# Kernel tuning notes

Measured on AMD Instinct MI355X. Metric: run time of the kernel, lower is better.

Reference implementation:

```python
import jax, jax.numpy as jnp
import numpy as np

N_X, N_UNITS, N_Y, N_U = 64, 256, 32, 64
BATCH = 32768


def setup_inputs() -> dict:
    key = jax.random.key(0)
    ks = jax.random.split(key, 10)
    nz = 2 * N_X + N_UNITS
    return {
        "u": jax.random.normal(ks[0], (BATCH, N_U, 1), dtype=jnp.float32),
        "x0": jax.random.normal(ks[1], (BATCH, N_X, 1), dtype=jnp.float32),
        # learned parameters (scaled down so H stays well-conditioned and tanh unsaturated)
        "B_2": 0.1 * jax.random.normal(ks[2], (N_X, N_U), dtype=jnp.float32),
        "C_2": 0.1 * jax.random.normal(ks[3], (N_Y, N_X), dtype=jnp.float32),
        "D_12": 0.1 * jax.random.normal(ks[4], (N_UNITS, N_U), dtype=jnp.float32),
        "D_21": 0.1 * jax.random.normal(ks[5], (N_Y, N_UNITS), dtype=jnp.float32),
        "b": 0.1 * jax.random.normal(ks[6], (N_X + N_UNITS + N_Y, 1), dtype=jnp.float32),
        "X": (1.0 / np.sqrt(nz)) * jax.random.normal(ks[7], (nz, nz), dtype=jnp.float32),
        "Y1": 0.1 * jax.random.normal(ks[8], (N_X, N_X), dtype=jnp.float32),
        # fixed IQC multipliers (train_qsr=False): Q nsd, R=I so Rinv=I; S stored transposed
        "S_t": 0.1 * jax.random.normal(ks[9], (N_U, N_Y), dtype=jnp.float32),
        "Q": -jnp.eye(N_Y, dtype=jnp.float32),
        "Rinv": jnp.eye(N_U, dtype=jnp.float32),
    }


def _constrained_weights(B_2, C_2, D_12, D_21, X, S_t, Q, Rinv):
    """Port of REN.updateConstrainedWeights (train_qsr=False). Returns C_1, D_11, lam."""
    n_x, n_units = B_2.shape[0], D_12.shape[0]
    n_y = C_2.shape[0]
    nz = 2 * n_x + n_units
    C2_ = S_t @ C_2                       # [n_u, n_x]
    D21_ = S_t @ D_21 - D_12.T            # [n_u, n_units]
    H = X.T @ X + 1e-3 * jnp.eye(nz, dtype=X.dtype)
    lT1 = jnp.concatenate([C2_.T, D21_.T, B_2], axis=0)          # [nz, n_u]
    H = H + lT1 @ Rinv @ lT1.T
    lT2 = jnp.concatenate([C_2.T, D_21.T, jnp.zeros((n_x, n_y), dtype=X.dtype)], axis=0)
    H = H - lT2 @ Q @ lT2.T
    H_21 = H[n_x:n_x + n_units, :n_x]
    H_22 = H[n_x:n_x + n_units, n_x:n_x + n_units]
    C_1 = -H_21                           # [n_units, n_x]
    lam = 0.5 * jnp.diag(H_22)            # Lambda diagonal, > 0 since H is PD
    # L = tril(-(H_22 - diag(H_22))) == -strictly_lower(H_22)
    D_11 = -jnp.tril(H_22, k=-1)          # strictly lower triangular [n_units, n_units]
    return C_1, D_11, lam


def _forward(u, x0, B_2, C_2, D_12, D_21, b, X, Y1, S_t, Q, Rinv):
    n_x, n_units = B_2.shape[0], D_12.shape[0]
    C_1, D_11, lam = _constrained_weights(B_2, C_2, D_12, D_21, X, S_t, Q, Rinv)
    u2 = u[:, :, 0]                       # [B, n_u]
    x2 = x0[:, :, 0]                      # [B, n_x]
    b_w = b[n_x:n_x + n_units, 0]         # [n_units]
    b_y = b[n_x + n_units:, 0]            # [n_y]
    # precompute the non-recurrent part of the pre-activation for all units
    v = x2 @ C_1.T + u2 @ D_12.T + b_w    # [B, n_units]
    # NOTE: the source uses D_11 row (i_unit - 1), not i_unit (faithful to original code).
    # For i=0 the source uses term2 = 0; D_11 is strictly lower so the full-row dot
    # against the partially-filled w (zeros beyond index i) matches D_11[i-1, :i] @ w[:i].
    Drows = jnp.concatenate([jnp.zeros((1, n_units), dtype=D_11.dtype), D_11[:-1]], axis=0)
    batch = u2.shape[0]

    def step(w, i):
        wi = jnp.tanh((v[:, i] + w @ Drows[i]) / lam[i])   # [B]
        w = w.at[:, i].set(wi)
        return w, None

    w0 = jnp.zeros((batch, n_units), dtype=v.dtype)
    w, _ = jax.lax.scan(step, w0, jnp.arange(n_units))
    y = x2 @ C_2.T + w @ D_21.T + b_y     # [B, n_y]
    return y[:, :, None]                  # [B, n_y, 1]


def reference(u, x0, B_2, C_2, D_12, D_21, b, X, Y1, S_t, Q, Rinv):
    return _forward(u, x0, B_2, C_2, D_12, D_21, b, X, Y1, S_t, Q, Rinv)
```

## Files before the change

kernel.cpp:

```cpp
#include <hip/hip_runtime.h>
#include <hip/hip_bf16.h>

typedef __attribute__((ext_vector_type(8))) short short8;
typedef __attribute__((ext_vector_type(4))) float floatx4;
typedef __attribute__((ext_vector_type(2))) float floatx2;

#define MFMA16 __builtin_amdgcn_mfma_f32_16x16x32_bf16

__device__ inline unsigned short bf16_rn(float f) {
    return (unsigned short)((__float_as_uint(f) + 0x8000u) >> 16);
}
__device__ inline short8 pack8(const float* v) {
    union { short8 s; unsigned int u[4]; } r;
#pragma unroll
    for (int j = 0; j < 4; j++) {
        union { __hip_bfloat162 h; unsigned int u; } c;
        c.h = __float22bfloat162_rn(make_float2(v[2 * j], v[2 * j + 1]));
        r.u[j] = c.u;
    }
    return r.s;
}

__global__ __launch_bounds__(64) void ren_prep13(
    const float* __restrict__ B2, const float* __restrict__ C2,
    const float* __restrict__ D12, const float* __restrict__ D21,
    const float* __restrict__ St, const float* __restrict__ Q,
    const float* __restrict__ Rinv,
    float* __restrict__ lT1, float* __restrict__ t1,
    float* __restrict__ lT2, float* __restrict__ t2,
    unsigned short* __restrict__ Wvb, unsigned short* __restrict__ C2b,
    unsigned short* __restrict__ D21b)
{
    const int t = threadIdx.x;
    const int blk = blockIdx.x;
    if (blk >= 384) {
        const int id = (blk - 384) * 64 + t;
        if (id < 16384) {
            Wvb[(id >> 6) * 128 + 64 + (id & 63)] = bf16_rn(D12[id]);
        } else if (id < 16384 + 2048) {
            C2b[id - 16384] = bf16_rn(C2[id - 16384]);
        } else if (id < 16384 + 2048 + 8192) {
            D21b[id - 18432] = bf16_rn(D21[id - 18432]);
        }
        return;
    }

    __shared__ float stl[64 * 33];
    __shared__ float colbuf[32];
    __shared__ float s1[64];

    const int r = blk;
    const int c = t;
#pragma unroll
    for (int j = 0; j < 32; j++) {
        const int id = j * 64 + t;
        stl[(id >> 5) * 33 + (id & 31)] = St[id];
    }
    if (t < 32)
        colbuf[t] = (r < 64) ? C2[t * 64 + r]
                  : (r < 320 ? D21[t * 256 + (r - 64)] : 0.f);
    __syncthreads();

    float v1;
    if (r < 64) {
        float s = 0.f;
#pragma unroll
        for (int p = 0; p < 32; p++) s += stl[c * 33 + p] * colbuf[p];
        v1 = s;
    } else if (r < 320) {
        float s = 0.f;
#pragma unroll
        for (int p = 0; p < 32; p++) s += stl[c * 33 + p] * colbuf[p];
        v1 = s - D12[(r - 64) * 64 + c];
    } else {
        v1 = B2[(r - 320) * 64 + c];
    }
    s1[c] = v1;
    lT1[r * 64 + c] = v1;
    if (c < 32) {
        const float v2 = (r < 320) ? colbuf[c] : 0.f;
        lT2[r * 32 + c] = v2;
    }
    __syncthreads();

    float a = 0.f;
#pragma unroll
    for (int k = 0; k < 64; k++) a += s1[k] * Rinv[k * 64 + c];
    t1[r * 64 + c] = a;

    if (c < 32) {
        float bq = 0.f;
#pragma unroll
        for (int k = 0; k < 32; k++) bq += colbuf[k] * Q[k * 32 + c];
        t2[r * 32 + c] = bq;
    }
}

__global__ __launch_bounds__(320) void ren_prep2(
    const float* __restrict__ X,
    const float* __restrict__ lT1, const float* __restrict__ t1,
    const float* __restrict__ lT2, const float* __restrict__ t2,
    unsigned short* __restrict__ Wvb, unsigned short* __restrict__ Drowsb,
    float* __restrict__ Dpair, float* __restrict__ lamg)
{
    __shared__ float xcol[384];
    const int c = threadIdx.x;
    const int i = blockIdx.x;
    for (int t = c; t < 384; t += 320) xcol[t] = X[t * 384 + 64 + i];
    __syncthreads();

    float f0 = 0.f, f1 = 0.f, f2 = 0.f, f3 = 0.f;
    float ac[8], au[8], bc8[8], bu[8];
#pragma unroll
    for (int kk = 0; kk < 8; kk++) { ac[kk] = X[kk * 384 + c]; au[kk] = xcol[kk]; }
    for (int k0 = 0; k0 < 384; k0 += 16) {
#pragma unroll
        for (int kk = 0; kk < 8; kk++) {
            bc8[kk] = X[(k0 + 8 + kk) * 384 + c]; bu[kk] = xcol[k0 + 8 + kk];
        }
        f0 += au[0] * ac[0]; f1 += au[1] * ac[1];
        f2 += au[2] * ac[2]; f3 += au[3] * ac[3];
        f0 += au[4] * ac[4]; f1 += au[5] * ac[5];
        f2 += au[6] * ac[6]; f3 += au[7] * ac[7];
        if (k0 + 16 < 384) {
#pragma unroll
            for (int kk = 0; kk < 8; kk++) {
                ac[kk] = X[(k0 + 16 + kk) * 384 + c]; au[kk] = xcol[k0 + 16 + kk];
            }
        }
        f0 += bu[0] * bc8[0]; f1 += bu[1] * bc8[1];
        f2 += bu[2] * bc8[2]; f3 += bu[3] * bc8[3];
        f0 += bu[4] * bc8[4]; f1 += bu[5] * bc8[5];
        f2 += bu[6] * bc8[6]; f3 += bu[7] * bc8[7];
    }

    const float* __restrict__ t1r = t1 + (64 + i) * 64;
    const float* __restrict__ l1r = lT1 + c * 64;
#pragma unroll
    for (int m4 = 0; m4 < 16; m4++) {
        const float4 lv = *(const float4*)(l1r + m4 * 4);
        f0 += t1r[m4 * 4 + 0] * lv.x; f1 += t1r[m4 * 4 + 1] * lv.y;
        f2 += t1r[m4 * 4 + 2] * lv.z; f3 += t1r[m4 * 4 + 3] * lv.w;
    }
    const float* __restrict__ t2r = t2 + (64 + i) * 32;
    const float* __restrict__ l2r = lT2 + c * 32;
#pragma unroll
    for (int m4 = 0; m4 < 8; m4++) {
        const float4 lv = *(const float4*)(l2r + m4 * 4);
        f0 -= t2r[m4 * 4 + 0] * lv.x; f1 -= t2r[m4 * 4 + 1] * lv.y;
        f2 -= t2r[m4 * 4 + 2] * lv.z; f3 -= t2r[m4 * 4 + 3] * lv.w;
    }
    float acc = (f0 + f1) + (f2 + f3) + (((64 + i) == c) ? 0.001f : 0.f);

    if (c < 64) {
        Wvb[i * 128 + c] = bf16_rn(-acc);
    } else {
        const int cb = c - 64;
        if (cb == i) lamg[i] = 5.7707801635558536f / acc;
        if (i < 255) {
            const float dv = (cb <= i - 1) ? -acc : 0.f;
            Drowsb[(i + 1) * 256 + cb] = bf16_rn(dv);
            const int row = i + 1;
            if ((row >> 4) == (cb >> 4)) {
                const int q = row & 15, p = cb & 15;
                Dpair[(row >> 4) * 256 + (q >> 1) * 32 + p * 2 + (q & 1)] = dv;
            }
        } else {
            Drowsb[cb] = 0;
        }
    }
}

__global__ __launch_bounds__(64) void ren_main(
    const float* __restrict__ u, const float* __restrict__ x0,
    const float* __restrict__ b,
    const unsigned short* __restrict__ Wvb,
    const unsigned short* __restrict__ Drowsb,
    const float* __restrict__ Dpair,
    const float* __restrict__ lamg,
    const unsigned short* __restrict__ C2b,
    const unsigned short* __restrict__ D21b,
    float* __restrict__ out)
{
    __shared__ float buf[16][20];
    __shared__ float dblk[256];
    __shared__ float lamsh[256];
    __shared__ float bsh[256];

    const int L = threadIdx.x;
    const int col = L & 15;
    const int quad = L >> 4;
    const int row0 = blockIdx.x * 16;

#pragma unroll
    for (int j = 0; j < 4; j++) {
        lamsh[j * 64 + L] = lamg[j * 64 + L];
        bsh[j * 64 + L]   = b[64 + j * 64 + L];
    }

    short8 zf[4];
#pragma unroll
    for (int c = 0; c < 4; c++) {
        const float* p = (c < 2 ? x0 : u) + (long)(row0 + col) * 64 + (c & 1) * 32 + quad * 8;
        float t[8];
        *(float4*)&t[0] = *(const float4*)p;
        *(float4*)&t[4] = *(const float4*)(p + 4);
        zf[c] = pack8(t);
    }

    const short8 zero8 = {0, 0, 0, 0, 0, 0, 0, 0};
    short8 wf[8];
#pragma unroll
    for (int c = 0; c < 8; c++) wf[c] = zero8;

    short8 vf[2][4], hf[2][8], yc[4];
    float4 dt = *(const float4*)(Dpair + 4 * L);
#pragma unroll
    for (int c = 0; c < 4; c++)
        vf[0][c] = *(const short8*)(Wvb + col * 128 + c * 32 + quad * 8);
#pragma unroll
    for (int c = 0; c < 8; c++) { hf[0][c] = zero8; hf[1][c] = zero8; }

#pragma unroll
    for (int n = 0; n < 16; n++) {
        const int cur = n & 1, nxt = cur ^ 1;

        *(float4*)&dblk[4 * L] = dt;

        if (n < 15) {
            dt = *(const float4*)(Dpair + (n + 1) * 256 + 4 * L);
#pragma unroll
            for (int c = 0; c < 4; c++)
                vf[nxt][c] = *(const short8*)(Wvb + (16 * (n + 1) + col) * 128 + c * 32 + quad * 8);
#pragma unroll
            for (int c = 0; c < 8; c++)
                if (c < ((n + 2) >> 1))
                    hf[nxt][c] = *(const short8*)(Drowsb + (16 * (n + 1) + col) * 256 + c * 32 + quad * 8);
        } else {
            yc[0] = *(const short8*)(C2b + col * 64 + quad * 8);
            yc[1] = *(const short8*)(C2b + col * 64 + 32 + quad * 8);
            yc[2] = *(const short8*)(C2b + (16 + col) * 64 + quad * 8);
            yc[3] = *(const short8*)(C2b + (16 + col) * 64 + 32 + quad * 8);
        }

        floatx4 acc0 = {0.f, 0.f, 0.f, 0.f}, acc1 = {0.f, 0.f, 0.f, 0.f};
        acc0 = MFMA16(zf[0], vf[cur][0], acc0, 0, 0, 0);
        acc1 = MFMA16(zf[1], vf[cur][1], acc1, 0, 0, 0);
        acc0 = MFMA16(zf[2], vf[cur][2], acc0, 0, 0, 0);
        acc1 = MFMA16(zf[3], vf[cur][3], acc1, 0, 0, 0);
#pragma unroll
        for (int c = 0; c < 8; c++)
            if (c < ((n + 1) >> 1)) {
                if (c & 1) acc1 = MFMA16(wf[c], hf[cur][c], acc1, 0, 0, 0);
                else       acc0 = MFMA16(wf[c], hf[cur][c], acc0, 0, 0, 0);
            }

        const float bwv = bsh[16 * n + col];
#pragma unroll
        for (int r = 0; r < 4; r++)
            buf[quad * 4 + r][col] = acc0[r] + acc1[r] + bwv;

        float vl[16];
#pragma unroll
        for (int p4 = 0; p4 < 4; p4++)
            *(float4*)&vl[p4 * 4] = *(const float4*)&buf[col][p4 * 4];

        float wl[16];
#pragma unroll
        for (int t = 0; t < 8; t++) {
            floatx2 a2;
            a2[0] = vl[2 * t]; a2[1] = vl[2 * t + 1];
#pragma unroll
            for (int p4 = 0; p4 < t; p4++) {
                const float4 d4 = *(const float4*)&dblk[t * 32 + p4 * 4];
                floatx2 de; de[0] = d4.x; de[1] = d4.y;
                floatx2 dz; dz[0] = d4.z; dz[1] = d4.w;
                a2 += de * wl[2 * p4];
                a2 += dz * wl[2 * p4 + 1];
            }
            const float2 lmp = *(const float2*)&lamsh[16 * n + 2 * t];
            floatx2 lm2; lm2[0] = lmp.x; lm2[1] = lmp.y;
            a2 *= lm2;
            const float e0 = __builtin_amdgcn_exp2f(a2[0]);
            const float e1 = __builtin_amdgcn_exp2f(a2[1]);
            wl[2 * t]     = 1.f - 2.f * __builtin_amdgcn_rcpf(e0 + 1.f);
            wl[2 * t + 1] = 1.f - 2.f * __builtin_amdgcn_rcpf(e1 + 1.f);
        }

        {
            const short8 nf = pack8(&wl[(quad & 1) * 8]);
            const int cc = n >> 1;
            if ((n & 1) == 0) wf[cc] = (quad < 2) ? nf : zero8;
            else if (quad >= 2) wf[cc] = nf;
        }
    }

    floatx4 y0 = {0.f, 0.f, 0.f, 0.f}, y1 = {0.f, 0.f, 0.f, 0.f};
    y0 = MFMA16(zf[0], yc[0], y0, 0, 0, 0);
    y1 = MFMA16(zf[0], yc[2], y1, 0, 0, 0);
    y0 = MFMA16(zf[1], yc[1], y0, 0, 0, 0);
    y1 = MFMA16(zf[1], yc[3], y1, 0, 0, 0);
#pragma unroll
    for (int c = 0; c < 8; c++) {
        const short8 b0 = *(const short8*)(D21b + col * 256 + c * 32 + quad * 8);
        const short8 b1 = *(const short8*)(D21b + (16 + col) * 256 + c * 32 + quad * 8);
        y0 = MFMA16(wf[c], b0, y0, 0, 0, 0);
        y1 = MFMA16(wf[c], b1, y1, 0, 0, 0);
    }
    const float by0 = b[320 + col];
    const float by1 = b[336 + col];
#pragma unroll
    for (int r = 0; r < 4; r++) {
        out[(long)(row0 + quad * 4 + r) * 32 + col]      = y0[r] + by0;
        out[(long)(row0 + quad * 4 + r) * 32 + 16 + col] = y1[r] + by1;
    }
}

extern "C" void kernel_launch(void* const* d_in, const int* in_sizes, int n_in,
                              void* d_out, int out_size, void* d_ws, size_t ws_size,
                              hipStream_t stream)
{
    const float* u    = (const float*)d_in[0];
    const float* x0   = (const float*)d_in[1];
    const float* B2   = (const float*)d_in[2];
    const float* C2   = (const float*)d_in[3];
    const float* D12  = (const float*)d_in[4];
    const float* D21  = (const float*)d_in[5];
    const float* b    = (const float*)d_in[6];
    const float* X    = (const float*)d_in[7];
    const float* St   = (const float*)d_in[9];
    const float* Q    = (const float*)d_in[10];
    const float* Rinv = (const float*)d_in[11];
    float* out = (float*)d_out;

    float* ws     = (float*)d_ws;
    float* lT1    = ws;
    float* t1     = lT1 + 384 * 64;
    float* lT2    = t1 + 384 * 64;
    float* t2     = lT2 + 384 * 32;
    float* lamg   = t2 + 384 * 32;
    float* Dpair  = lamg + 256;
    unsigned short* Drowsb = (unsigned short*)(Dpair + 16 * 256);
    unsigned short* Wvb    = Drowsb + 256 * 256;
    unsigned short* C2b    = Wvb + 256 * 128;
    unsigned short* D21b   = C2b + 32 * 64;

    ren_prep13<<<dim3(800), dim3(64), 0, stream>>>(B2, C2, D12, D21, St, Q, Rinv,
                                                   lT1, t1, lT2, t2, Wvb, C2b, D21b);
    ren_prep2<<<dim3(256), dim3(320), 0, stream>>>(X, lT1, t1, lT2, t2,
                                                   Wvb, Drowsb, Dpair, lamg);

    const int batch = in_sizes[0] / 64;
    ren_main<<<dim3(batch / 16), dim3(64), 0, stream>>>(u, x0, b, Wvb, Drowsb,
                                                        Dpair, lamg, C2b, D21b, out);
}
```

Baseline: 142.2 us.

## Compute next block's MFMA pre-activation at end of iteration with double-buffered LDS

Restructures the 16-block recurrence so each block's MFMA pre-activation is computed at the end of the previous iteration, right after the new w fragment is packed. Block 0's input projection moves before the loop. The LDS scratch buffers (buf, dblk) are double-buffered by iteration parity, so writes for the next block cannot clash with reads from the current one. The aim is to shorten the per-block dependency chain and let MFMA and load latency overlap with the scalar tanh triangle solve, at the cost of more LDS and register pressure.

```diff
diff --git a/kernel.cpp b/kernel.cpp
--- a/kernel.cpp
+++ b/kernel.cpp
@@ -182,8 +182,8 @@
     const unsigned short* __restrict__ D21b,
     float* __restrict__ out)
 {
-    __shared__ float buf[16][20];
-    __shared__ float dblk[256];
+    __shared__ float buf[2][16][20];
+    __shared__ float dblk[2][256];
     __shared__ float lamsh[256];
     __shared__ float bsh[256];
 
@@ -213,29 +213,36 @@
 #pragma unroll
     for (int c = 0; c < 8; c++) wf[c] = zero8;
 
-    short8 vf[2][4], hf[2][8], yc[4];
-    float4 dt = *(const float4*)(Dpair + 4 * L);
-#pragma unroll
-    for (int c = 0; c < 4; c++)
-        vf[0][c] = *(const short8*)(Wvb + col * 128 + c * 32 + quad * 8);
-#pragma unroll
-    for (int c = 0; c < 8; c++) { hf[0][c] = zero8; hf[1][c] = zero8; }
+    float4 dcur = *(const float4*)(Dpair + 4 * L);
+    floatx4 acc0 = {0.f, 0.f, 0.f, 0.f}, acc1 = {0.f, 0.f, 0.f, 0.f};
+    {
+        short8 v0 = *(const short8*)(Wvb + col * 128 + quad * 8);
+        short8 v1 = *(const short8*)(Wvb + col * 128 + 32 + quad * 8);
+        short8 v2 = *(const short8*)(Wvb + col * 128 + 64 + quad * 8);
+        short8 v3 = *(const short8*)(Wvb + col * 128 + 96 + quad * 8);
+        acc0 = MFMA16(zf[0], v0, acc0, 0, 0, 0);
+        acc1 = MFMA16(zf[1], v1, acc1, 0, 0, 0);
+        acc0 = MFMA16(zf[2], v2, acc0, 0, 0, 0);
+        acc1 = MFMA16(zf[3], v3, acc1, 0, 0, 0);
+    }
+
+    short8 yc[4];
 
 #pragma unroll
     for (int n = 0; n < 16; n++) {
-        const int cur = n & 1, nxt = cur ^ 1;
-
-        *(float4*)&dblk[4 * L] = dt;
-
+        const int pp = n & 1;
+
+        short8 vfN[4], hfN[8];
+        float4 dnxt;
         if (n < 15) {
-            dt = *(const float4*)(Dpair + (n + 1) * 256 + 4 * L);
+            dnxt = *(const float4*)(Dpair + (n + 1) * 256 + 4 * L);
 #pragma unroll
             for (int c = 0; c < 4; c++)
-                vf[nxt][c] = *(const short8*)(Wvb + (16 * (n + 1) + col) * 128 + c * 32 + quad * 8);
+                vfN[c] = *(const short8*)(Wvb + (16 * (n + 1) + col) * 128 + c * 32 + quad * 8);
 #pragma unroll
             for (int c = 0; c < 8; c++)
                 if (c < ((n + 2) >> 1))
-                    hf[nxt][c] = *(const short8*)(Drowsb + (16 * (n + 1) + col) * 256 + c * 32 + quad * 8);
+                    hfN[c] = *(const short8*)(Drowsb + (16 * (n + 1) + col) * 256 + c * 32 + quad * 8);
         } else {
             yc[0] = *(const short8*)(C2b + col * 64 + quad * 8);
             yc[1] = *(const short8*)(C2b + col * 64 + 32 + quad * 8);
@@ -243,48 +250,37 @@
             yc[3] = *(const short8*)(C2b + (16 + col) * 64 + 32 + quad * 8);
         }
 
-        floatx4 acc0 = {0.f, 0.f, 0.f, 0.f}, acc1 = {0.f, 0.f, 0.f, 0.f};
-        acc0 = MFMA16(zf[0], vf[cur][0], acc0, 0, 0, 0);
-        acc1 = MFMA16(zf[1], vf[cur][1], acc1, 0, 0, 0);
-        acc0 = MFMA16(zf[2], vf[cur][2], acc0, 0, 0, 0);
-        acc1 = MFMA16(zf[3], vf[cur][3], acc1, 0, 0, 0);
-#pragma unroll
-        for (int c = 0; c < 8; c++)
-            if (c < ((n + 1) >> 1)) {
-                if (c & 1) acc1 = MFMA16(wf[c], hf[cur][c], acc1, 0, 0, 0);
-                else       acc0 = MFMA16(wf[c], hf[cur][c], acc0, 0, 0, 0);
-            }
-
+        *(float4*)&dblk[pp][4 * L] = dcur;
         const float bwv = bsh[16 * n + col];
 #pragma unroll
         for (int r = 0; r < 4; r++)
-            buf[quad * 4 + r][col] = acc0[r] + acc1[r] + bwv;
+            buf[pp][quad * 4 + r][col] = acc0[r] + acc1[r] + bwv;
 
         float vl[16];
 #pragma unroll
         for (int p4 = 0; p4 < 4; p4++)
-            *(float4*)&vl[p4 * 4] = *(const float4*)&buf[col][p4 * 4];
+            *(float4*)&vl[p4 * 4] = *(const float4*)&buf[pp][col][p4 * 4];
 
         float wl[16];
 #pragma unroll
-        for (int t = 0; t < 8; t++) {
+        for (int tq = 0; tq < 8; tq++) {
             floatx2 a2;
-            a2[0] = vl[2 * t]; a2[1] = vl[2 * t + 1];
-#pragma unroll
-            for (int p4 = 0; p4 < t; p4++) {
-                const float4 d4 = *(const float4*)&dblk[t * 32 + p4 * 4];
+            a2[0] = vl[2 * tq]; a2[1] = vl[2 * tq + 1];
+#pragma unroll
+            for (int p4 = 0; p4 < tq; p4++) {
+                const float4 d4 = *(const float4*)&dblk[pp][tq * 32 + p4 * 4];
                 floatx2 de; de[0] = d4.x; de[1] = d4.y;
                 floatx2 dz; dz[0] = d4.z; dz[1] = d4.w;
                 a2 += de * wl[2 * p4];
                 a2 += dz * wl[2 * p4 + 1];
             }
-            const float2 lmp = *(const float2*)&lamsh[16 * n + 2 * t];
+            const float2 lmp = *(const float2*)&lamsh[16 * n + 2 * tq];
             floatx2 lm2; lm2[0] = lmp.x; lm2[1] = lmp.y;
             a2 *= lm2;
             const float e0 = __builtin_amdgcn_exp2f(a2[0]);
             const float e1 = __builtin_amdgcn_exp2f(a2[1]);
-            wl[2 * t]     = 1.f - 2.f * __builtin_amdgcn_rcpf(e0 + 1.f);
-            wl[2 * t + 1] = 1.f - 2.f * __builtin_amdgcn_rcpf(e1 + 1.f);
+            wl[2 * tq]     = 1.f - 2.f * __builtin_amdgcn_rcpf(e0 + 1.f);
+            wl[2 * tq + 1] = 1.f - 2.f * __builtin_amdgcn_rcpf(e1 + 1.f);
         }
 
         {
@@ -292,6 +288,22 @@
             const int cc = n >> 1;
             if ((n & 1) == 0) wf[cc] = (quad < 2) ? nf : zero8;
             else if (quad >= 2) wf[cc] = nf;
+        }
+
+        if (n < 15) {
+            floatx4 a0 = {0.f, 0.f, 0.f, 0.f}, a1 = {0.f, 0.f, 0.f, 0.f};
+            a0 = MFMA16(zf[0], vfN[0], a0, 0, 0, 0);
+            a1 = MFMA16(zf[1], vfN[1], a1, 0, 0, 0);
+            a0 = MFMA16(zf[2], vfN[2], a0, 0, 0, 0);
+            a1 = MFMA16(zf[3], vfN[3], a1, 0, 0, 0);
+#pragma unroll
+            for (int c = 0; c < 8; c++)
+                if (c < ((n + 2) >> 1)) {
+                    if (c & 1) a1 = MFMA16(wf[c], hfN[c], a1, 0, 0, 0);
+                    else       a0 = MFMA16(wf[c], hfN[c], a0, 0, 0, 0);
+                }
+            acc0 = a0; acc1 = a1;
+            dcur = dnxt;
         }
     }
 
```

New measurement: 141.3 us. Within noise of the previous version (-0.6%).
